# Kernel tuning notes

Measured on AMD Instinct MI355X. Metric: run time of the kernel, lower is better.

Reference implementation:

```python
import jax, jax.numpy as jnp
import numpy as np

EPS_POS = 0.65
EPS_NEG = 0.4
TAU = 0.03
TEMPERATURE = 0.07


def setup_inputs() -> dict:
    key = jax.random.key(0)
    k1, k2 = jax.random.split(key)
    N, H, W, C = 256, 14, 14, 512  # ResNet18 layer4 features (448x448 frame), pooled audio
    frame = jax.random.normal(k1, (N, H, W, C), dtype=jnp.float32)
    audio = jax.random.normal(k2, (N, C), dtype=jnp.float32)
    return {"frame": frame, "audio": audio}


def reference(frame, audio):
    # frame: [N, H, W, C] vision backbone features; audio: [N, C] pooled audio embedding
    N = frame.shape[0]
    f = frame * jax.lax.rsqrt(jnp.sum(frame * frame, axis=3, keepdims=True))  # l2_normalize axis=3
    a = audio * jax.lax.rsqrt(jnp.sum(audio * audio, axis=1, keepdims=True))  # l2_normalize axis=1

    # S_ii: per-sample spatial similarity map [N, 1, H, W]
    S_ii = jnp.einsum('nhwc,nc->nhw', f, a)[:, None, :, :]
    # S_ij: cross-batch similarity [N, K, H, W] (K == N)
    S_ij = jnp.einsum('nhwc,kc->nkhw', f, a)

    m_ip = jax.nn.sigmoid((S_ii - EPS_POS) / TAU)   # positive soft-mask
    neg = 1.0 - jax.nn.sigmoid((S_ii - EPS_NEG) / TAU)  # hard-negative soft-mask

    # Pi: masked mean of positive similarities -> [N, 1]
    Pi = jnp.sum(m_ip * S_ii, axis=(2, 3)) / jnp.sum(m_ip, axis=(2, 3))

    n_all = jax.nn.sigmoid((S_ij - EPS_POS) / TAU)
    mask = 1.0 - 100.0 * jnp.eye(N, dtype=frame.dtype)  # kill diagonal (self) pairs
    Ni_easy = (jnp.sum(n_all * S_ij, axis=(2, 3)) / jnp.sum(n_all, axis=(2, 3))) * mask  # [N, N]
    Ni_hard = jnp.sum(neg * S_ii, axis=(2, 3)) / jnp.sum(neg, axis=(2, 3))  # [N, 1]

    data = jnp.concatenate([Pi, Ni_hard, Ni_easy], axis=1) * TEMPERATURE  # [N, N+2]

    # __calc_loss (faithful to TF broadcasting: Pi_d is [N,1], Ni_d is [N] -> [N,N] broadcast)
    Pi_d = data[:, 0:1]
    Ni_d = jnp.sum(data[:, 1:], axis=1)
    Pi_e = jnp.exp(Pi_d)
    Ni_e = jnp.exp(Ni_d)
    loss = (-1.0 / N) * jnp.sum(jnp.log(Pi_e / (Pi_e + Ni_e)))
    return loss
```

## Files before the change

### kernel.cpp

```cpp
#include <hip/hip_runtime.h>
#include <stdint.h>

#define N_IMG 256
#define HW 196
#define CDIM 512

#define F_EPS_POS 0.65f
#define F_EPS_NEG 0.40f
#define F_INV_TAU (1.0f/0.03f)
#define F_TEMP 0.07f

typedef __attribute__((ext_vector_type(8))) short bf16x8;
typedef __attribute__((ext_vector_type(8))) unsigned short u16x8;
typedef __attribute__((ext_vector_type(4))) float f32x4;

__device__ __forceinline__ unsigned short f2bf(float x){
    unsigned int u = __float_as_uint(x);
    u = (u + 0x7FFFu + ((u >> 16) & 1u)) >> 16;
    return (unsigned short)u;
}
__device__ __forceinline__ float sigm(float x){ return 1.0f/(1.0f + __expf(-x)); }

__global__ void audio_norm_k(const float* __restrict__ audio,
                             unsigned short* __restrict__ abf){
    int k = blockIdx.x, t = threadIdx.x;
    __shared__ float red[256];
    float v0 = audio[k*CDIM + t];
    float v1 = audio[k*CDIM + t + 256];
    red[t] = v0*v0 + v1*v1;
    __syncthreads();
    for (int s = 128; s > 0; s >>= 1){
        if (t < s) red[t] += red[t+s];
        __syncthreads();
    }
    float rrt = 1.0f / sqrtf(red[0]);
    abf[k*CDIM + t]       = f2bf(v0*rrt);
    abf[k*CDIM + t + 256] = f2bf(v1*rrt);
}

__global__ __launch_bounds__(256, 4)
void main_k(const float* __restrict__ frame,
            const unsigned short* __restrict__ abf,
            float* __restrict__ num, float* __restrict__ den,
            float* __restrict__ hnum, float* __restrict__ hden){
    __shared__ unsigned short fT[2][16*520];
    __shared__ float rnormS[2][16];

    const int t = threadIdx.x;
    const int w  = ((blockIdx.x & 7) << 7) + (blockIdx.x >> 3);
    const int n  = w >> 2;
    const int k0 = (w & 3) << 6;
    const int lane = t & 63, wid = t >> 6;
    const int col  = lane & 15, quad = lane >> 4;
    const int kg   = k0 + wid*16 + col;

    bf16x8 B[16];
    {
        const unsigned short* bp = abf + (size_t)kg*CDIM + quad*8;
        #pragma unroll
        for (int j = 0; j < 16; ++j) B[j] = *(const bf16x8*)(bp + j*32);
    }

    const int r = t >> 4;
    const int c = t & 15;

    float en = 0.f, ed = 0.f, hn = 0.f, hd = 0.f;

    auto loadT = [&](int pt, float4* v){
        int p = pt*16 + r;
        if (p > HW-1) p = HW-1;
        const float4* src = (const float4*)(frame + ((size_t)n*HW + p)*CDIM);
        #pragma unroll
        for (int i = 0; i < 8; ++i)
            v[i] = src[(c << 1) + (i & 1) + (i >> 1)*32];
    };
    auto storeT = [&](const float4* v, int buf){
        float ss = 0.f;
        #pragma unroll
        for (int i = 0; i < 8; ++i)
            ss += v[i].x*v[i].x + v[i].y*v[i].y + v[i].z*v[i].z + v[i].w*v[i].w;
        unsigned short* dst = fT[buf] + r*520 + c*8;
        #pragma unroll
        for (int j = 0; j < 4; ++j){
            float4 a = v[2*j], b = v[2*j+1];
            u16x8 u = { f2bf(a.x), f2bf(a.y), f2bf(a.z), f2bf(a.w),
                        f2bf(b.x), f2bf(b.y), f2bf(b.z), f2bf(b.w) };
            *(u16x8*)(dst + j*128) = u;
        }
        ss += __shfl_xor(ss, 1, 64);
        ss += __shfl_xor(ss, 2, 64);
        ss += __shfl_xor(ss, 4, 64);
        ss += __shfl_xor(ss, 8, 64);
        if (c == 0)
            rnormS[buf][r] = (ss > 0.f) ? (1.0f/sqrtf(ss)) : 0.f;
    };

    {
        float4 v[8];
        loadT(0, v);
        storeT(v, 0);
    }
    __syncthreads();

    for (int pt = 0; pt < 13; ++pt){
        const int cur = pt & 1, nxt = cur ^ 1;
        const bool hasNext = (pt < 12);

        float4 v[8];
        if (hasNext) loadT(pt + 1, v);

        const unsigned short* fbase = fT[cur] + col*520 + quad*8;
        f32x4 acc = {0.f,0.f,0.f,0.f};
        #pragma unroll
        for (int j = 0; j < 16; ++j){
            bf16x8 a = *(const bf16x8*)(fbase + j*32);
            acc = __builtin_amdgcn_mfma_f32_16x16x32_bf16(a, B[j], acc, 0, 0, 0);
        }
        f32x4 rn4 = *(const f32x4*)(&rnormS[cur][quad*4]);
        #pragma unroll
        for (int rr = 0; rr < 4; ++rr){
            int prow = pt*16 + quad*4 + rr;
            if (prow < HW){
                float s  = acc[rr] * rn4[rr];
                float wp = sigm((s - F_EPS_POS) * F_INV_TAU);
                en += wp*s; ed += wp;
                if (kg == n){ float wn = 1.f - sigm((s - F_EPS_NEG) * F_INV_TAU); hn += wn*s; hd += wn; }
            }
        }

        if (hasNext) storeT(v, nxt);
        __syncthreads();
    }

    en += __shfl_xor(en, 16, 64); en += __shfl_xor(en, 32, 64);
    ed += __shfl_xor(ed, 16, 64); ed += __shfl_xor(ed, 32, 64);
    hn += __shfl_xor(hn, 16, 64); hn += __shfl_xor(hn, 32, 64);
    hd += __shfl_xor(hd, 16, 64); hd += __shfl_xor(hd, 32, 64);

    if (quad == 0){
        num[n*N_IMG + kg] = en;  den[n*N_IMG + kg] = ed;
        if (kg == n){ hnum[n] = hn; hden[n] = hd; }
    }
}

__global__ void pd_k(const float* __restrict__ num, const float* __restrict__ den,
                     const float* __restrict__ hnum, const float* __restrict__ hden,
                     float* __restrict__ Pi_d, float* __restrict__ Ni_d){
    int nn = blockIdx.x, t = threadIdx.x;
    __shared__ float red[256];
    __shared__ float diagv;
    float ratio = num[nn*N_IMG + t] / den[nn*N_IMG + t];
    if (t == nn) diagv = ratio;
    red[t] = ratio * (t == nn ? -99.f : 1.f);
    __syncthreads();
    for (int s = 128; s > 0; s >>= 1){
        if (t < s) red[t] += red[t+s];
        __syncthreads();
    }
    if (t == 0){
        Pi_d[nn] = F_TEMP * diagv;
        Ni_d[nn] = F_TEMP * (hnum[nn]/hden[nn] + red[0]);
    }
}

__global__ void loss_k(const float* __restrict__ Pi_d, const float* __restrict__ Ni_d,
                       float* __restrict__ out){
    int i = blockIdx.x, j = threadIdx.x;
    __shared__ float red[256];
    float x = Ni_d[j] - Pi_d[i];
    red[j] = (x > 20.f) ? x : log1pf(__expf(x));
    __syncthreads();
    for (int s = 128; s > 0; s >>= 1){
        if (j < s) red[j] += red[j+s];
        __syncthreads();
    }
    if (j == 0) atomicAdd(out, red[0] * (1.0f/(float)N_IMG));
}

extern "C" void kernel_launch(void* const* d_in, const int* in_sizes, int n_in,
                              void* d_out, int out_size, void* d_ws, size_t ws_size,
                              hipStream_t stream) {
    const float* frame = (const float*)d_in[0];
    const float* audio = (const float*)d_in[1];
    float* out = (float*)d_out;
    char* ws = (char*)d_ws;

    unsigned short* abf = (unsigned short*)(ws);
    float* num  = (float*)(ws + 262144);
    float* den  = (float*)(ws + 524288);
    float* hnum = (float*)(ws + 786432);
    float* hden = (float*)(ws + 787456);
    float* Pi_d = (float*)(ws + 788480);
    float* Ni_d = (float*)(ws + 789504);

    hipMemsetAsync(out, 0, sizeof(float), stream);

    audio_norm_k<<<N_IMG, 256, 0, stream>>>(audio, abf);
    main_k<<<N_IMG*4, 256, 0, stream>>>(frame, abf, num, den, hnum, hden);
    pd_k<<<N_IMG, 256, 0, stream>>>(num, den, hnum, hden, Pi_d, Ni_d);
    loss_k<<<N_IMG, 256, 0, stream>>>(Pi_d, Ni_d, out);
}
```

Before: 195.0 us.

## Use one 1024-thread block per image to share frame tiles across all audio columns

The main kernel now launches one 1024-thread block per image covering all 256 audio rows, instead of four 256-thread blocks that each reloaded and re-converted the same frame tiles. Each wavefront loads one spatial row with fully coalesced float4 reads and computes its norm with a full-wave shuffle reduction. The tile loop is manually unrolled with a two-stage register prefetch to overlap global loads with MFMA work. The trade-off is fewer, larger blocks with higher register pressure per CU and less scheduling flexibility.

```diff
diff --git a/kernel.cpp b/kernel.cpp
--- a/kernel.cpp
+++ b/kernel.cpp
@@ -11,7 +11,7 @@
 #define F_TEMP 0.07f
 
 typedef __attribute__((ext_vector_type(8))) short bf16x8;
-typedef __attribute__((ext_vector_type(8))) unsigned short u16x8;
+typedef __attribute__((ext_vector_type(4))) unsigned short u16x4;
 typedef __attribute__((ext_vector_type(4))) float f32x4;
 
 __device__ __forceinline__ unsigned short f2bf(float x){
@@ -38,7 +38,7 @@
     abf[k*CDIM + t + 256] = f2bf(v1*rrt);
 }
 
-__global__ __launch_bounds__(256, 4)
+__global__ __launch_bounds__(1024, 4)
 void main_k(const float* __restrict__ frame,
             const unsigned short* __restrict__ abf,
             float* __restrict__ num, float* __restrict__ den,
@@ -46,13 +46,11 @@
     __shared__ unsigned short fT[2][16*520];
     __shared__ float rnormS[2][16];
 
-    const int t = threadIdx.x;
-    const int w  = ((blockIdx.x & 7) << 7) + (blockIdx.x >> 3);
-    const int n  = w >> 2;
-    const int k0 = (w & 3) << 6;
+    const int t    = threadIdx.x;
+    const int n    = blockIdx.x;
     const int lane = t & 63, wid = t >> 6;
     const int col  = lane & 15, quad = lane >> 4;
-    const int kg   = k0 + wid*16 + col;
+    const int kg   = wid*16 + col;
 
     bf16x8 B[16];
     {
@@ -61,76 +59,80 @@
         for (int j = 0; j < 16; ++j) B[j] = *(const bf16x8*)(bp + j*32);
     }
 
-    const int r = t >> 4;
-    const int c = t & 15;
-
     float en = 0.f, ed = 0.f, hn = 0.f, hd = 0.f;
 
+    const float4* fbase_g = (const float4*)(frame + (size_t)n*HW*CDIM);
+
     auto loadT = [&](int pt, float4* v){
-        int p = pt*16 + r;
-        if (p > HW-1) p = HW-1;
-        const float4* src = (const float4*)(frame + ((size_t)n*HW + p)*CDIM);
-        #pragma unroll
-        for (int i = 0; i < 8; ++i)
-            v[i] = src[(c << 1) + (i & 1) + (i >> 1)*32];
+        int p = pt*16 + wid; if (p > HW-1) p = HW-1;
+        const float4* s = fbase_g + (size_t)p*(CDIM/4);
+        v[0] = s[lane];
+        v[1] = s[lane + 64];
     };
     auto storeT = [&](const float4* v, int buf){
-        float ss = 0.f;
+        float ss = v[0].x*v[0].x + v[0].y*v[0].y + v[0].z*v[0].z + v[0].w*v[0].w
+                 + v[1].x*v[1].x + v[1].y*v[1].y + v[1].z*v[1].z + v[1].w*v[1].w;
+        unsigned short* d = fT[buf] + wid*520;
+        u16x4 u0 = { f2bf(v[0].x), f2bf(v[0].y), f2bf(v[0].z), f2bf(v[0].w) };
+        u16x4 u1 = { f2bf(v[1].x), f2bf(v[1].y), f2bf(v[1].z), f2bf(v[1].w) };
+        *(u16x4*)(d + lane*4)       = u0;
+        *(u16x4*)(d + 256 + lane*4) = u1;
         #pragma unroll
-        for (int i = 0; i < 8; ++i)
-            ss += v[i].x*v[i].x + v[i].y*v[i].y + v[i].z*v[i].z + v[i].w*v[i].w;
-        unsigned short* dst = fT[buf] + r*520 + c*8;
-        #pragma unroll
-        for (int j = 0; j < 4; ++j){
-            float4 a = v[2*j], b = v[2*j+1];
-            u16x8 u = { f2bf(a.x), f2bf(a.y), f2bf(a.z), f2bf(a.w),
-                        f2bf(b.x), f2bf(b.y), f2bf(b.z), f2bf(b.w) };
-            *(u16x8*)(dst + j*128) = u;
-        }
-        ss += __shfl_xor(ss, 1, 64);
-        ss += __shfl_xor(ss, 2, 64);
-        ss += __shfl_xor(ss, 4, 64);
-        ss += __shfl_xor(ss, 8, 64);
-        if (c == 0)
-            rnormS[buf][r] = (ss > 0.f) ? (1.0f/sqrtf(ss)) : 0.f;
+        for (int dd = 1; dd < 64; dd <<= 1) ss += __shfl_xor(ss, dd, 64);
+        if (lane == 0)
+            rnormS[buf][wid] = (ss > 0.f) ? (1.0f/sqrtf(ss)) : 0.f;
     };
 
-    {
-        float4 v[8];
-        loadT(0, v);
-        storeT(v, 0);
-    }
-    __syncthreads();
-
-    for (int pt = 0; pt < 13; ++pt){
-        const int cur = pt & 1, nxt = cur ^ 1;
-        const bool hasNext = (pt < 12);
-
-        float4 v[8];
-        if (hasNext) loadT(pt + 1, v);
-
-        const unsigned short* fbase = fT[cur] + col*520 + quad*8;
-        f32x4 acc = {0.f,0.f,0.f,0.f};
-        #pragma unroll
-        for (int j = 0; j < 16; ++j){
-            bf16x8 a = *(const bf16x8*)(fbase + j*32);
-            acc = __builtin_amdgcn_mfma_f32_16x16x32_bf16(a, B[j], acc, 0, 0, 0);
-        }
-        f32x4 rn4 = *(const f32x4*)(&rnormS[cur][quad*4]);
-        #pragma unroll
-        for (int rr = 0; rr < 4; ++rr){
-            int prow = pt*16 + quad*4 + rr;
-            if (prow < HW){
-                float s  = acc[rr] * rn4[rr];
-                float wp = sigm((s - F_EPS_POS) * F_INV_TAU);
-                en += wp*s; ed += wp;
-                if (kg == n){ float wn = 1.f - sigm((s - F_EPS_NEG) * F_INV_TAU); hn += wn*s; hd += wn; }
-            }
-        }
-
-        if (hasNext) storeT(v, nxt);
-        __syncthreads();
-    }
+    float4 vA[2], vB[2];
+
+    loadT(0, vA);
+    storeT(vA, 0);
+    loadT(1, vA);
+    __syncthreads();
+
+#define BODY(PT, P, Q) do{                                                     \
+    if ((PT)+2 < 13) loadT((PT)+2, Q);                                         \
+    {                                                                          \
+        const unsigned short* fb = fT[(PT)&1] + col*520 + quad*8;              \
+        f32x4 acc = {0.f,0.f,0.f,0.f};                                         \
+        _Pragma("unroll")                                                      \
+        for (int j = 0; j < 16; ++j){                                          \
+            bf16x8 a = *(const bf16x8*)(fb + j*32);                            \
+            acc = __builtin_amdgcn_mfma_f32_16x16x32_bf16(a, B[j], acc, 0,0,0);\
+        }                                                                      \
+        f32x4 rn4 = *(const f32x4*)(&rnormS[(PT)&1][quad*4]);                  \
+        _Pragma("unroll")                                                      \
+        for (int rr = 0; rr < 4; ++rr){                                        \
+            int prow = (PT)*16 + quad*4 + rr;                                  \
+            if (prow < HW){                                                    \
+                float s  = acc[rr] * rn4[rr];                                  \
+                float wp = sigm((s - F_EPS_POS) * F_INV_TAU);                  \
+                en += wp*s; ed += wp;                                          \
+                if (kg == n){                                                  \
+                    float wn = 1.f - sigm((s - F_EPS_NEG) * F_INV_TAU);        \
+                    hn += wn*s; hd += wn;                                      \
+                }                                                              \
+            }                                                                  \
+        }                                                                      \
+    }                                                                          \
+    if ((PT)+1 < 13) storeT(P, ((PT)+1)&1);                                    \
+    __syncthreads();                                                           \
+}while(0)
+
+    BODY(0,  vA, vB);
+    BODY(1,  vB, vA);
+    BODY(2,  vA, vB);
+    BODY(3,  vB, vA);
+    BODY(4,  vA, vB);
+    BODY(5,  vB, vA);
+    BODY(6,  vA, vB);
+    BODY(7,  vB, vA);
+    BODY(8,  vA, vB);
+    BODY(9,  vB, vA);
+    BODY(10, vA, vB);
+    BODY(11, vB, vA);
+    BODY(12, vA, vB);
+#undef BODY
 
     en += __shfl_xor(en, 16, 64); en += __shfl_xor(en, 32, 64);
     ed += __shfl_xor(ed, 16, 64); ed += __shfl_xor(ed, 32, 64);
@@ -196,7 +198,7 @@
     hipMemsetAsync(out, 0, sizeof(float), stream);
 
     audio_norm_k<<<N_IMG, 256, 0, stream>>>(audio, abf);
-    main_k<<<N_IMG*4, 256, 0, stream>>>(frame, abf, num, den, hnum, hden);
+    main_k<<<N_IMG, 1024, 0, stream>>>(frame, abf, num, den, hnum, hden);
     pd_k<<<N_IMG, 256, 0, stream>>>(num, den, hnum, hden, Pi_d, Ni_d);
     loss_k<<<N_IMG, 256, 0, stream>>>(Pi_d, Ni_d, out);
 }
```

Result: faster. 185.9 us (-4.7%).
